# Performance work log

Hardware: AMD Instinct MI355X
Metric: run time of the kernel (lower is better)

Reference implementation:

```python
import jax, jax.numpy as jnp
import numpy as np

EPS = 1e-5

def setup_inputs() -> dict:
    key = jax.random.key(0)
    k1, k2 = jax.random.split(key, 2)
    B, S, D = 4, 4096, 4096
    x = jax.random.normal(k1, (B, S, D), dtype=jnp.float32)
    mask = jax.random.bernoulli(k2, 0.5, (B, S, D))  # BackRazor activation mask
    weight = jnp.ones((D,), dtype=jnp.float32)
    return {"x": x, "mask": mask, "weight": weight}

def reference(x, mask, weight):
    # sparsify -> unsparsify round-trip == zero out unmasked activations
    xm = jnp.where(mask, x, jnp.zeros((), dtype=x.dtype))
    # RMS variance in float32, as in the original
    variance = jnp.mean(jnp.square(xm.astype(jnp.float32)), axis=-1, keepdims=True)
    x_norm = xm * jax.lax.rsqrt(variance + EPS)
    return weight * x_norm
```

## Files before the change

kernel.cpp:

```cpp
#include <hip/hip_runtime.h>


#define EPS_RMS 1e-5f

__global__ void detect_mask_kernel(const unsigned char* __restrict__ mb,
                                   int* __restrict__ flag) {
    __shared__ int nz_off;
    __shared__ int f3;
    if (threadIdx.x == 0) { nz_off = 0; f3 = 0; }
    __syncthreads();
    unsigned int i = threadIdx.x * 4u;
    unsigned char b1 = mb[i + 1], b2 = mb[i + 2], b3 = mb[i + 3];
    if ((b1 | b2 | b3) != 0) atomicOr(&nz_off, 1);
    if (b3 == 0x3fu) atomicOr(&f3, 1);
    __syncthreads();
    if (threadIdx.x == 0) {
        *flag = f3 ? 2 : (nz_off ? 0 : 1);
    }
}

__global__ __launch_bounds__(256) void rmsnorm_sparse_4096(
    const float* __restrict__ x,
    const void* __restrict__ mask,
    const float* __restrict__ weight,
    float* __restrict__ out,
    const int* __restrict__ flag_p) {
    const int D = 4096;
    const int row = blockIdx.x;
    const int t = threadIdx.x;
    const int flag = *flag_p;
    const size_t base = (size_t)row * (size_t)D;

    const float4* __restrict__ x4 = (const float4*)(x + base);
    float4* __restrict__ o4 = (float4*)(out + base);
    const float4* __restrict__ w4 = (const float4*)weight;

    float4 v[4];

    if (flag == 0) {
        const uchar4* m4 = (const uchar4*)((const unsigned char*)mask + base);
#pragma unroll
        for (int i = 0; i < 4; ++i) {
            const int idx = t + i * 256;
            float4 xv = x4[idx];
            uchar4 u = m4[idx];
            xv.x = u.x ? xv.x : 0.f;
            xv.y = u.y ? xv.y : 0.f;
            xv.z = u.z ? xv.z : 0.f;
            xv.w = u.w ? xv.w : 0.f;
            v[i] = xv;
        }
    } else if (flag == 1) {
        const int4* m4 = (const int4*)((const int*)mask + base);
#pragma unroll
        for (int i = 0; i < 4; ++i) {
            const int idx = t + i * 256;
            float4 xv = x4[idx];
            int4 u = m4[idx];
            xv.x = u.x ? xv.x : 0.f;
            xv.y = u.y ? xv.y : 0.f;
            xv.z = u.z ? xv.z : 0.f;
            xv.w = u.w ? xv.w : 0.f;
            v[i] = xv;
        }
    } else {
        const float4* m4 = (const float4*)((const float*)mask + base);
#pragma unroll
        for (int i = 0; i < 4; ++i) {
            const int idx = t + i * 256;
            float4 xv = x4[idx];
            float4 u = m4[idx];
            xv.x = (u.x != 0.f) ? xv.x : 0.f;
            xv.y = (u.y != 0.f) ? xv.y : 0.f;
            xv.z = (u.z != 0.f) ? xv.z : 0.f;
            xv.w = (u.w != 0.f) ? xv.w : 0.f;
            v[i] = xv;
        }
    }

    float s = 0.f;
#pragma unroll
    for (int i = 0; i < 4; ++i) {
        s += v[i].x * v[i].x + v[i].y * v[i].y + v[i].z * v[i].z +
             v[i].w * v[i].w;
    }
#pragma unroll
    for (int off = 32; off > 0; off >>= 1) s += __shfl_down(s, off);

    __shared__ float ws[4];
    const int lane = t & 63;
    const int wave = t >> 6;
    if (lane == 0) ws[wave] = s;
    __syncthreads();
    const float total = ws[0] + ws[1] + ws[2] + ws[3];
    const float scale = rsqrtf(total * (1.0f / (float)D) + EPS_RMS);

#pragma unroll
    for (int i = 0; i < 4; ++i) {
        const int idx = t + i * 256;
        float4 w = w4[idx];
        float4 o;
        o.x = v[i].x * scale * w.x;
        o.y = v[i].y * scale * w.y;
        o.z = v[i].z * scale * w.z;
        o.w = v[i].w * scale * w.w;
        o4[idx] = o;
    }
}

__global__ void rmsnorm_sparse_generic(const float* __restrict__ x,
                                       const void* __restrict__ mask,
                                       const float* __restrict__ weight,
                                       float* __restrict__ out,
                                       const int* __restrict__ flag_p, int D) {
    const int row = blockIdx.x;
    const int t = threadIdx.x;
    const int flag = *flag_p;
    const size_t base = (size_t)row * (size_t)D;

    float s = 0.f;
    for (int d = t; d < D; d += blockDim.x) {
        float xv = x[base + d];
        bool m;
        if (flag == 0)
            m = ((const unsigned char*)mask)[base + d] != 0;
        else if (flag == 1)
            m = ((const int*)mask)[base + d] != 0;
        else
            m = ((const float*)mask)[base + d] != 0.f;
        float xm = m ? xv : 0.f;
        s += xm * xm;
    }
#pragma unroll
    for (int off = 32; off > 0; off >>= 1) s += __shfl_down(s, off);
    __shared__ float ws[16];
    const int lane = t & 63;
    const int wave = t >> 6;
    if (lane == 0) ws[wave] = s;
    __syncthreads();
    float total = 0.f;
    const int nw = (blockDim.x + 63) / 64;
    for (int i = 0; i < nw; ++i) total += ws[i];
    const float scale = rsqrtf(total / (float)D + EPS_RMS);

    for (int d = t; d < D; d += blockDim.x) {
        float xv = x[base + d];
        bool m;
        if (flag == 0)
            m = ((const unsigned char*)mask)[base + d] != 0;
        else if (flag == 1)
            m = ((const int*)mask)[base + d] != 0;
        else
            m = ((const float*)mask)[base + d] != 0.f;
        float xm = m ? xv : 0.f;
        out[base + d] = weight[d] * xm * scale;
    }
}

extern "C" void kernel_launch(void* const* d_in, const int* in_sizes, int n_in,
                              void* d_out, int out_size, void* d_ws,
                              size_t ws_size, hipStream_t stream) {
    const float* x = (const float*)d_in[0];
    const void* mask = d_in[1];
    const float* weight = (const float*)d_in[2];
    float* out = (float*)d_out;

    const int D = in_sizes[2];
    const int rows = in_sizes[0] / D;

    int* flag = (int*)d_ws;
    detect_mask_kernel<<<1, 256, 0, stream>>>((const unsigned char*)mask, flag);

    if (D == 4096) {
        rmsnorm_sparse_4096<<<rows, 256, 0, stream>>>(x, mask, weight, out,
                                                      flag);
    } else {
        rmsnorm_sparse_generic<<<rows, 256, 0, stream>>>(x, mask, weight, out,
                                                         flag, D);
    }
}
```

Baseline: 148.0 us.

## Map one wavefront per row to drop LDS reduction and block barrier

Each 64-lane wavefront now handles a whole 4096-element row, four rows per 256-thread block. The cross-wave shared-memory reduction and __syncthreads are replaced by a butterfly shuffle within the wave, loads are batched 16-deep per lane, and outputs use nontemporal stores. This raises per-thread register use (16 float4 values plus masks) in exchange for more memory-level parallelism and less synchronization. The int and float mask paths re-read their inputs in a second pass instead of keeping them in registers.

```diff
diff --git a/kernel.cpp b/kernel.cpp
--- a/kernel.cpp
+++ b/kernel.cpp
@@ -2,6 +2,8 @@
 
 
 #define EPS_RMS 1e-5f
+
+typedef float f32x4 __attribute__((ext_vector_type(4)));
 
 __global__ void detect_mask_kernel(const unsigned char* __restrict__ mb,
                                    int* __restrict__ flag) {
@@ -19,92 +21,99 @@
     }
 }
 
-__global__ __launch_bounds__(256) void rmsnorm_sparse_4096(
+__global__ __launch_bounds__(256) void rmsnorm_sparse_wave4096(
     const float* __restrict__ x,
     const void* __restrict__ mask,
     const float* __restrict__ weight,
     float* __restrict__ out,
-    const int* __restrict__ flag_p) {
-    const int D = 4096;
-    const int row = blockIdx.x;
-    const int t = threadIdx.x;
+    const int* __restrict__ flag_p,
+    int nrows) {
+    const int lane = threadIdx.x & 63;
+    const int row = blockIdx.x * 4 + (threadIdx.x >> 6);
+    if (row >= nrows) return;
+
     const int flag = *flag_p;
-    const size_t base = (size_t)row * (size_t)D;
-
-    const float4* __restrict__ x4 = (const float4*)(x + base);
-    float4* __restrict__ o4 = (float4*)(out + base);
-    const float4* __restrict__ w4 = (const float4*)weight;
-
-    float4 v[4];
+    const size_t base = (size_t)row * 4096u;
+    const f32x4* __restrict__ x4 = (const f32x4*)(x + base);
+    const f32x4* __restrict__ w4 = (const f32x4*)weight;
+    f32x4* __restrict__ o4 = (f32x4*)(out + base);
 
     if (flag == 0) {
-        const uchar4* m4 = (const uchar4*)((const unsigned char*)mask + base);
+        const uchar4* __restrict__ m4 =
+            (const uchar4*)((const unsigned char*)mask + base);
+        f32x4 v[16];
 #pragma unroll
-        for (int i = 0; i < 4; ++i) {
-            const int idx = t + i * 256;
-            float4 xv = x4[idx];
-            uchar4 u = m4[idx];
+        for (int w = 0; w < 16; ++w) v[w] = x4[lane + 64 * w];
+        uchar4 mm[16];
+#pragma unroll
+        for (int w = 0; w < 16; ++w) mm[w] = m4[lane + 64 * w];
+
+        float s = 0.f;
+#pragma unroll
+        for (int w = 0; w < 16; ++w) {
+            f32x4 xv = v[w];
+            const uchar4 u = mm[w];
             xv.x = u.x ? xv.x : 0.f;
             xv.y = u.y ? xv.y : 0.f;
             xv.z = u.z ? xv.z : 0.f;
             xv.w = u.w ? xv.w : 0.f;
-            v[i] = xv;
+            v[w] = xv;
+            s += xv.x * xv.x + xv.y * xv.y + xv.z * xv.z + xv.w * xv.w;
         }
-    } else if (flag == 1) {
-        const int4* m4 = (const int4*)((const int*)mask + base);
 #pragma unroll
-        for (int i = 0; i < 4; ++i) {
-            const int idx = t + i * 256;
-            float4 xv = x4[idx];
-            int4 u = m4[idx];
-            xv.x = u.x ? xv.x : 0.f;
-            xv.y = u.y ? xv.y : 0.f;
-            xv.z = u.z ? xv.z : 0.f;
-            xv.w = u.w ? xv.w : 0.f;
-            v[i] = xv;
+        for (int off = 1; off < 64; off <<= 1) s += __shfl_xor(s, off);
+        const float scale = rsqrtf(s * (1.0f / 4096.0f) + EPS_RMS);
+
+#pragma unroll
+        for (int w = 0; w < 16; ++w) {
+            const f32x4 wv = w4[lane + 64 * w];
+            const f32x4 o = v[w] * (scale)*wv;
+            __builtin_nontemporal_store(o, &o4[lane + 64 * w]);
         }
     } else {
-        const float4* m4 = (const float4*)((const float*)mask + base);
+        float s = 0.f;
+        if (flag == 1) {
+            const int4* m4 = (const int4*)((const int*)mask + base);
+            for (int w = 0; w < 16; ++w) {
+                const f32x4 xv = x4[lane + 64 * w];
+                const int4 u = m4[lane + 64 * w];
+                s += (u.x ? xv.x * xv.x : 0.f) + (u.y ? xv.y * xv.y : 0.f) +
+                     (u.z ? xv.z * xv.z : 0.f) + (u.w ? xv.w * xv.w : 0.f);
+            }
+        } else {
+            const f32x4* m4 = (const f32x4*)((const float*)mask + base);
+            for (int w = 0; w < 16; ++w) {
+                const f32x4 xv = x4[lane + 64 * w];
+                const f32x4 u = m4[lane + 64 * w];
+                s += (u.x != 0.f ? xv.x * xv.x : 0.f) +
+                     (u.y != 0.f ? xv.y * xv.y : 0.f) +
+                     (u.z != 0.f ? xv.z * xv.z : 0.f) +
+                     (u.w != 0.f ? xv.w * xv.w : 0.f);
+            }
+        }
 #pragma unroll
-        for (int i = 0; i < 4; ++i) {
-            const int idx = t + i * 256;
-            float4 xv = x4[idx];
-            float4 u = m4[idx];
-            xv.x = (u.x != 0.f) ? xv.x : 0.f;
-            xv.y = (u.y != 0.f) ? xv.y : 0.f;
-            xv.z = (u.z != 0.f) ? xv.z : 0.f;
-            xv.w = (u.w != 0.f) ? xv.w : 0.f;
-            v[i] = xv;
+        for (int off = 1; off < 64; off <<= 1) s += __shfl_xor(s, off);
+        const float scale = rsqrtf(s * (1.0f / 4096.0f) + EPS_RMS);
+
+        for (int w = 0; w < 16; ++w) {
+            f32x4 xv = x4[lane + 64 * w];
+            if (flag == 1) {
+                const int4 u = ((const int4*)((const int*)mask + base))[lane + 64 * w];
+                xv.x = u.x ? xv.x : 0.f;
+                xv.y = u.y ? xv.y : 0.f;
+                xv.z = u.z ? xv.z : 0.f;
+                xv.w = u.w ? xv.w : 0.f;
+            } else {
+                const f32x4 u =
+                    ((const f32x4*)((const float*)mask + base))[lane + 64 * w];
+                xv.x = (u.x != 0.f) ? xv.x : 0.f;
+                xv.y = (u.y != 0.f) ? xv.y : 0.f;
+                xv.z = (u.z != 0.f) ? xv.z : 0.f;
+                xv.w = (u.w != 0.f) ? xv.w : 0.f;
+            }
+            const f32x4 wv = w4[lane + 64 * w];
+            o4[lane + 64 * w] = xv * scale * wv;
         }
-    }
-
-    float s = 0.f;
-#pragma unroll
-    for (int i = 0; i < 4; ++i) {
-        s += v[i].x * v[i].x + v[i].y * v[i].y + v[i].z * v[i].z +
-             v[i].w * v[i].w;
-    }
-#pragma unroll
-    for (int off = 32; off > 0; off >>= 1) s += __shfl_down(s, off);
-
-    __shared__ float ws[4];
-    const int lane = t & 63;
-    const int wave = t >> 6;
-    if (lane == 0) ws[wave] = s;
-    __syncthreads();
-    const float total = ws[0] + ws[1] + ws[2] + ws[3];
-    const float scale = rsqrtf(total * (1.0f / (float)D) + EPS_RMS);
-
-#pragma unroll
-    for (int i = 0; i < 4; ++i) {
-        const int idx = t + i * 256;
-        float4 w = w4[idx];
-        float4 o;
-        o.x = v[i].x * scale * w.x;
-        o.y = v[i].y * scale * w.y;
-        o.z = v[i].z * scale * w.z;
-        o.w = v[i].w * scale * w.w;
-        o4[idx] = o;
     }
 }
 
@@ -172,8 +181,9 @@
     detect_mask_kernel<<<1, 256, 0, stream>>>((const unsigned char*)mask, flag);
 
     if (D == 4096) {
-        rmsnorm_sparse_4096<<<rows, 256, 0, stream>>>(x, mask, weight, out,
-                                                      flag);
+        const int blocks = (rows + 3) / 4;
+        rmsnorm_sparse_wave4096<<<blocks, 256, 0, stream>>>(x, mask, weight,
+                                                            out, flag, rows);
     } else {
         rmsnorm_sparse_generic<<<rows, 256, 0, stream>>>(x, mask, weight, out,
                                                          flag, D);
```

After: 224.1 us. +51.4%, slower.

## Use persistent blocks with next-row prefetch for the byte-mask RMSNorm path

Applied to the files above, without the earlier changes.

The D=4096 kernel becomes a persistent grid-stride kernel capped at 2048 blocks. Each block loads weight once and software-pipelines row loads, prefetching the next row's x and mask while it reduces and writes the current row. The row-sum barrier is replaced with a raw s_barrier over double-buffered shared slots. The fast kernel now handles only byte masks, and a second generic launch covers the other mask formats, which adds an extra launch that exits early and more register pressure from the prefetch buffers.

```diff
diff --git a/kernel.cpp b/kernel.cpp
--- a/kernel.cpp
+++ b/kernel.cpp
@@ -2,6 +2,8 @@
 
 
 #define EPS_RMS 1e-5f
+
+typedef float f32x4 __attribute__((ext_vector_type(4)));
 
 __global__ void detect_mask_kernel(const unsigned char* __restrict__ mb,
                                    int* __restrict__ flag) {
@@ -19,92 +21,89 @@
     }
 }
 
-__global__ __launch_bounds__(256) void rmsnorm_sparse_4096(
+__global__ __launch_bounds__(256, 4) void rmsnorm_sparse_fast4096(
     const float* __restrict__ x,
-    const void* __restrict__ mask,
+    const unsigned char* __restrict__ mask,
     const float* __restrict__ weight,
     float* __restrict__ out,
-    const int* __restrict__ flag_p) {
-    const int D = 4096;
-    const int row = blockIdx.x;
+    const int* __restrict__ flag_p,
+    int nrows, int rstride) {
+    if (*flag_p != 0) return;
+
     const int t = threadIdx.x;
-    const int flag = *flag_p;
-    const size_t base = (size_t)row * (size_t)D;
+    __shared__ float ws[2][4];
 
-    const float4* __restrict__ x4 = (const float4*)(x + base);
-    float4* __restrict__ o4 = (float4*)(out + base);
-    const float4* __restrict__ w4 = (const float4*)weight;
+    const f32x4* __restrict__ w4 = (const f32x4*)weight;
+    f32x4 wv[4];
+#pragma unroll
+    for (int i = 0; i < 4; ++i) wv[i] = w4[t + 256 * i];
 
-    float4 v[4];
+    const f32x4* __restrict__ x4 = (const f32x4*)x;
+    const uchar4* __restrict__ m4 = (const uchar4*)mask;
+    f32x4* __restrict__ o4 = (f32x4*)out;
 
-    if (flag == 0) {
-        const uchar4* m4 = (const uchar4*)((const unsigned char*)mask + base);
+    int r = blockIdx.x;
+    if (r >= nrows) return;
+
+    f32x4 xv[4];
+    uchar4 mm[4];
+    {
+        const size_t b = (size_t)r * 1024u;
+#pragma unroll
+        for (int i = 0; i < 4; ++i) xv[i] = x4[b + t + 256 * i];
+#pragma unroll
+        for (int i = 0; i < 4; ++i) mm[i] = m4[b + t + 256 * i];
+    }
+
+    int parity = 0;
+    for (;;) {
+        const int rn = r + rstride;
+        const bool has_next = rn < nrows;
+
+        f32x4 xn[4];
+        uchar4 mn[4];
+        if (has_next) {
+            const size_t nb = (size_t)rn * 1024u;
+#pragma unroll
+            for (int i = 0; i < 4; ++i) xn[i] = x4[nb + t + 256 * i];
+#pragma unroll
+            for (int i = 0; i < 4; ++i) mn[i] = m4[nb + t + 256 * i];
+        }
+
+        float s = 0.f;
+        f32x4 v[4];
 #pragma unroll
         for (int i = 0; i < 4; ++i) {
-            const int idx = t + i * 256;
-            float4 xv = x4[idx];
-            uchar4 u = m4[idx];
-            xv.x = u.x ? xv.x : 0.f;
-            xv.y = u.y ? xv.y : 0.f;
-            xv.z = u.z ? xv.z : 0.f;
-            xv.w = u.w ? xv.w : 0.f;
-            v[i] = xv;
+            f32x4 a = xv[i];
+            const uchar4 u = mm[i];
+            a.x = u.x ? a.x : 0.f;
+            a.y = u.y ? a.y : 0.f;
+            a.z = u.z ? a.z : 0.f;
+            a.w = u.w ? a.w : 0.f;
+            v[i] = a;
+            s += a.x * a.x + a.y * a.y + a.z * a.z + a.w * a.w;
         }
-    } else if (flag == 1) {
-        const int4* m4 = (const int4*)((const int*)mask + base);
 #pragma unroll
-        for (int i = 0; i < 4; ++i) {
-            const int idx = t + i * 256;
-            float4 xv = x4[idx];
-            int4 u = m4[idx];
-            xv.x = u.x ? xv.x : 0.f;
-            xv.y = u.y ? xv.y : 0.f;
-            xv.z = u.z ? xv.z : 0.f;
-            xv.w = u.w ? xv.w : 0.f;
-            v[i] = xv;
-        }
-    } else {
-        const float4* m4 = (const float4*)((const float*)mask + base);
+        for (int off = 1; off < 64; off <<= 1) s += __shfl_xor(s, off);
+
+        if ((t & 63) == 0) ws[parity][t >> 6] = s;
+        asm volatile("s_waitcnt lgkmcnt(0)" ::: "memory");
+        __builtin_amdgcn_s_barrier();
+        asm volatile("" ::: "memory");
+
+        const float total =
+            ws[parity][0] + ws[parity][1] + ws[parity][2] + ws[parity][3];
+        const float scale = rsqrtf(total * (1.0f / 4096.0f) + EPS_RMS);
+
+        const size_t ob = (size_t)r * 1024u;
 #pragma unroll
-        for (int i = 0; i < 4; ++i) {
-            const int idx = t + i * 256;
-            float4 xv = x4[idx];
-            float4 u = m4[idx];
-            xv.x = (u.x != 0.f) ? xv.x : 0.f;
-            xv.y = (u.y != 0.f) ? xv.y : 0.f;
-            xv.z = (u.z != 0.f) ? xv.z : 0.f;
-            xv.w = (u.w != 0.f) ? xv.w : 0.f;
-            v[i] = xv;
-        }
-    }
+        for (int i = 0; i < 4; ++i) o4[ob + t + 256 * i] = v[i] * scale * wv[i];
 
-    float s = 0.f;
+        if (!has_next) break;
+        r = rn;
 #pragma unroll
-    for (int i = 0; i < 4; ++i) {
-        s += v[i].x * v[i].x + v[i].y * v[i].y + v[i].z * v[i].z +
-             v[i].w * v[i].w;
-    }
-#pragma unroll
-    for (int off = 32; off > 0; off >>= 1) s += __shfl_down(s, off);
-
-    __shared__ float ws[4];
-    const int lane = t & 63;
-    const int wave = t >> 6;
-    if (lane == 0) ws[wave] = s;
-    __syncthreads();
-    const float total = ws[0] + ws[1] + ws[2] + ws[3];
-    const float scale = rsqrtf(total * (1.0f / (float)D) + EPS_RMS);
-
-#pragma unroll
-    for (int i = 0; i < 4; ++i) {
-        const int idx = t + i * 256;
-        float4 w = w4[idx];
-        float4 o;
-        o.x = v[i].x * scale * w.x;
-        o.y = v[i].y * scale * w.y;
-        o.z = v[i].z * scale * w.z;
-        o.w = v[i].w * scale * w.w;
-        o4[idx] = o;
+        for (int i = 0; i < 4; ++i) { xv[i] = xn[i]; mm[i] = mn[i]; }
+        parity ^= 1;
     }
 }
 
@@ -112,48 +111,54 @@
                                        const void* __restrict__ mask,
                                        const float* __restrict__ weight,
                                        float* __restrict__ out,
-                                       const int* __restrict__ flag_p, int D) {
-    const int row = blockIdx.x;
+                                       const int* __restrict__ flag_p, int D,
+                                       int nrows, int require_nonzero_flag) {
+    const int flag = *flag_p;
+    if (require_nonzero_flag && flag == 0) return;
+
     const int t = threadIdx.x;
-    const int flag = *flag_p;
-    const size_t base = (size_t)row * (size_t)D;
-
-    float s = 0.f;
-    for (int d = t; d < D; d += blockDim.x) {
-        float xv = x[base + d];
-        bool m;
-        if (flag == 0)
-            m = ((const unsigned char*)mask)[base + d] != 0;
-        else if (flag == 1)
-            m = ((const int*)mask)[base + d] != 0;
-        else
-            m = ((const float*)mask)[base + d] != 0.f;
-        float xm = m ? xv : 0.f;
-        s += xm * xm;
-    }
-#pragma unroll
-    for (int off = 32; off > 0; off >>= 1) s += __shfl_down(s, off);
-    __shared__ float ws[16];
     const int lane = t & 63;
     const int wave = t >> 6;
-    if (lane == 0) ws[wave] = s;
-    __syncthreads();
-    float total = 0.f;
     const int nw = (blockDim.x + 63) / 64;
-    for (int i = 0; i < nw; ++i) total += ws[i];
-    const float scale = rsqrtf(total / (float)D + EPS_RMS);
+    __shared__ float ws[16];
 
-    for (int d = t; d < D; d += blockDim.x) {
-        float xv = x[base + d];
-        bool m;
-        if (flag == 0)
-            m = ((const unsigned char*)mask)[base + d] != 0;
-        else if (flag == 1)
-            m = ((const int*)mask)[base + d] != 0;
-        else
-            m = ((const float*)mask)[base + d] != 0.f;
-        float xm = m ? xv : 0.f;
-        out[base + d] = weight[d] * xm * scale;
+    for (int row = blockIdx.x; row < nrows; row += gridDim.x) {
+        const size_t base = (size_t)row * (size_t)D;
+
+        float s = 0.f;
+        for (int d = t; d < D; d += blockDim.x) {
+            float xv = x[base + d];
+            bool m;
+            if (flag == 0)
+                m = ((const unsigned char*)mask)[base + d] != 0;
+            else if (flag == 1)
+                m = ((const int*)mask)[base + d] != 0;
+            else
+                m = ((const float*)mask)[base + d] != 0.f;
+            float xm = m ? xv : 0.f;
+            s += xm * xm;
+        }
+#pragma unroll
+        for (int off = 32; off > 0; off >>= 1) s += __shfl_down(s, off);
+        if (lane == 0) ws[wave] = s;
+        __syncthreads();
+        float total = 0.f;
+        for (int i = 0; i < nw; ++i) total += ws[i];
+        const float scale = rsqrtf(total / (float)D + EPS_RMS);
+        __syncthreads();
+
+        for (int d = t; d < D; d += blockDim.x) {
+            float xv = x[base + d];
+            bool m;
+            if (flag == 0)
+                m = ((const unsigned char*)mask)[base + d] != 0;
+            else if (flag == 1)
+                m = ((const int*)mask)[base + d] != 0;
+            else
+                m = ((const float*)mask)[base + d] != 0.f;
+            float xm = m ? xv : 0.f;
+            out[base + d] = weight[d] * xm * scale;
+        }
     }
 }
 
@@ -172,10 +177,14 @@
     detect_mask_kernel<<<1, 256, 0, stream>>>((const unsigned char*)mask, flag);
 
     if (D == 4096) {
-        rmsnorm_sparse_4096<<<rows, 256, 0, stream>>>(x, mask, weight, out,
-                                                      flag);
+        const int blocks = rows < 2048 ? rows : 2048;
+        rmsnorm_sparse_fast4096<<<blocks, 256, 0, stream>>>(
+            x, (const unsigned char*)mask, weight, out, flag, rows, blocks);
+        rmsnorm_sparse_generic<<<blocks, 256, 0, stream>>>(
+            x, mask, weight, out, flag, D, rows, 1);
     } else {
-        rmsnorm_sparse_generic<<<rows, 256, 0, stream>>>(x, mask, weight, out,
-                                                         flag, D);
+        const int blocks = rows < 2048 ? rows : 2048;
+        rmsnorm_sparse_generic<<<blocks, 256, 0, stream>>>(
+            x, mask, weight, out, flag, D, rows, 0);
     }
 }
```

Result: slower. 265.9 us (+79.6%).
